# Kernel optimization log

Hardware: AMD Instinct MI355X
Metric: run time of the kernel (lower is better)

Reference implementation:

```python
import jax, jax.numpy as jnp
import numpy as np

D_MODEL = 1024
NUM_HEADS = 16

def _dense_params(key, d_in, d_out):
    kw, _ = jax.random.split(key)
    # flax default: lecun_normal kernel, zeros bias
    W = jax.random.normal(kw, (d_in, d_out), dtype=jnp.float32) / np.sqrt(d_in)
    b = jnp.zeros((d_out,), dtype=jnp.float32)
    return W, b

def setup_inputs() -> dict:
    key = jax.random.key(0)
    ks = jax.random.split(key, 8)
    B, Tx, Tc = 2, 2048, 2048
    x = jax.random.normal(ks[0], (B, Tx, D_MODEL), dtype=jnp.float32)
    context = jax.random.normal(ks[1], (B, Tc, D_MODEL), dtype=jnp.float32)
    Wq, bq = _dense_params(ks[2], D_MODEL, D_MODEL)
    Wks, bks = _dense_params(ks[3], D_MODEL, D_MODEL)
    Wvs, bvs = _dense_params(ks[4], D_MODEL, D_MODEL)
    Wkc, bkc = _dense_params(ks[5], D_MODEL, D_MODEL)
    Wvc, bvc = _dense_params(ks[6], D_MODEL, D_MODEL)
    Wo, bo = _dense_params(ks[7], D_MODEL, D_MODEL)
    return {"x": x, "context": context,
            "Wq": Wq, "bq": bq, "Wks": Wks, "bks": bks, "Wvs": Wvs, "bvs": bvs,
            "Wkc": Wkc, "bkc": bkc, "Wvc": Wvc, "bvc": bvc, "Wo": Wo, "bo": bo}

def _split_heads(t, H):
    B, T, C = t.shape
    return t.reshape(B, T, H, C // H).transpose(0, 2, 1, 3)  # [B,H,T,hd]

def reference(x, context, Wq, bq, Wks, bks, Wvs, bvs, Wkc, bkc, Wvc, bvc, Wo, bo):
    H = NUM_HEADS
    head_dim = D_MODEL // H
    q = x @ Wq + bq
    k = jnp.concatenate([x @ Wks + bks, context @ Wkc + bkc], axis=1)
    v = jnp.concatenate([x @ Wvs + bvs, context @ Wvc + bvc], axis=1)
    q = _split_heads(q, H)  # [B,H,Tq,hd]
    k = _split_heads(k, H)  # [B,H,Tk,hd]
    v = _split_heads(v, H)
    attn = jnp.einsum('bhqd,bhkd->bhqk', q, k) / jnp.sqrt(jnp.float32(head_dim))
    attn = jax.nn.softmax(attn, axis=-1)
    out = jnp.einsum('bhqk,bhkd->bhqd', attn, v)
    B, _, Tq, _ = out.shape
    out = out.transpose(0, 2, 1, 3).reshape(B, Tq, D_MODEL)
    return out @ Wo + bo
```

## Files before the change

kernel.cpp:

```cpp
#include <hip/hip_runtime.h>
#include <hip/hip_bf16.h>
#include <math.h>


typedef _Float16 f16;
typedef _Float16 f16x8 __attribute__((ext_vector_type(8)));
typedef _Float16 f16x4v __attribute__((ext_vector_type(4)));
typedef float    f32x4 __attribute__((ext_vector_type(4)));

#define MFMA_F16(a, b, c) __builtin_amdgcn_mfma_f32_16x16x32_f16((a), (b), (c), 0, 0, 0)

#define QSCALE 0.18033688011112042f

__device__ __forceinline__ void glds16(const f16* g, f16* l) {
    __builtin_amdgcn_global_load_lds(
        (const __attribute__((address_space(1))) void*)g,
        (__attribute__((address_space(3))) void*)l, 16, 0, 0);
}

__global__ __launch_bounds__(256) void prep(
    const float4* __restrict__ x, const float4* __restrict__ ctx,
    f16x4v* __restrict__ xb, f16x4v* __restrict__ cb,
    const float* __restrict__ W0, const float* __restrict__ W1,
    const float* __restrict__ W2, const float* __restrict__ W3,
    const float* __restrict__ W4, const float* __restrict__ W5,
    f16* __restrict__ wt)
{
    if (blockIdx.x < 8192) {
        const int n4 = (2 * 2048 * 1024) / 4;
        int i = blockIdx.x * 256 + threadIdx.x;
        float4 v;
        f16x4v* dst;
        if (i < n4) { v = x[i];        dst = xb + i; }
        else        { v = ctx[i - n4]; dst = cb + (i - n4); }
        f16x4v h = { (f16)v.x, (f16)v.y, (f16)v.z, (f16)v.w };
        *dst = h;
        return;
    }
    const int idx = blockIdx.x - 8192;
    const int z = idx >> 10, rem = idx & 1023;
    const float* Ws[6] = { W0, W1, W2, W3, W4, W5 };
    const float* W = Ws[z];
    f16* Wt = wt + (size_t)z * (1024 * 1024);

    __shared__ float tile[32][33];
    const int tx = threadIdx.x & 31, ty = threadIdx.x >> 5;
    const int n0 = (rem & 31) * 32, k0 = (rem >> 5) * 32;

#pragma unroll
    for (int i = 0; i < 4; ++i) {
        int r = i * 8 + ty;
        tile[r][tx] = W[(size_t)(k0 + r) * 1024 + n0 + tx];
    }
    __syncthreads();
#pragma unroll
    for (int i = 0; i < 4; ++i) {
        int r = i * 8 + ty;
        Wt[(size_t)(n0 + r) * 1024 + k0 + tx] = (f16)tile[tx][r];
    }
}

#define GEMM_PROLOGUE(BN)                                                     \
    const int m0 = blockIdx.x * 128, n0 = blockIdx.y * (BN);                  \
    const int tid = threadIdx.x;                                              \
    const int w = tid >> 6, lane = tid & 63, quad = lane >> 4, l15 = lane & 15;\
    const int wm = (w >> 1) * 64, wn = (w & 1) * ((BN) / 2);                  \
    const int qsw = (quad ^ ((l15 >> 1) & 3)) * 8;                            \
    int gA[2], gB[(BN) / 64];                                                 \
    _Pragma("unroll")                                                         \
    for (int p = 0; p < 2; ++p) {                                             \
        int s = tid + p * 256;                                                \
        int r = (s >> 2) & 127, c = (s & 3) ^ ((s >> 3) & 3);                 \
        gA[p] = (m0 + r) * 1024 + c * 8;                                      \
    }                                                                         \
    _Pragma("unroll")                                                         \
    for (int p = 0; p < (BN) / 64; ++p) {                                     \
        int s = tid + p * 256;                                                \
        int r = (s >> 2) & ((BN) - 1), c = (s & 3) ^ ((s >> 3) & 3);          \
        gB[p] = (n0 + r) * 1024 + c * 8;                                      \
    }

#define GEMM_STAGE(BN)                                                        \
    __syncthreads();                                                          \
    _Pragma("unroll")                                                         \
    for (int p = 0; p < 2; ++p) glds16(&A[gA[p] + k0], &As[(p * 256 + w * 64) * 8]); \
    _Pragma("unroll")                                                         \
    for (int p = 0; p < (BN) / 64; ++p) glds16(&Bt[gB[p] + k0], &Bs[(p * 256 + w * 64) * 8]); \
    __syncthreads();

__global__ __launch_bounds__(256) void proj_gemm(
    const f16* __restrict__ xb, const f16* __restrict__ cb,
    const f16* __restrict__ wt,
    const float* __restrict__ bq, const float* __restrict__ bks,
    const float* __restrict__ bkc, const float* __restrict__ bvs,
    const float* __restrict__ bvc,
    f16* __restrict__ qbuf, f16* __restrict__ kbuf, f16* __restrict__ vbuf)
{
    __shared__ alignas(16) f16 As[128 * 32];
    __shared__ alignas(16) f16 Bs[128 * 32];

    const int z = blockIdx.z;
    const f16* A = (z == 0 || z == 1 || z == 3) ? xb : cb;
    const int wslot = (z == 0) ? 0 : (z == 1) ? 1 : (z == 2) ? 3 : (z == 3) ? 2 : 4;
    const f16* Bt = wt + (size_t)wslot * 1048576;
    const float* bias = (z == 0) ? bq : (z == 1) ? bks : (z == 2) ? bkc
                        : (z == 3) ? bvs : bvc;
    const int roff = (z == 2 || z == 4) ? 2048 : 0;

    GEMM_PROLOGUE(128)
    f32x4 acc[4][4] = {};

    for (int k0 = 0; k0 < 1024; k0 += 32) {
        GEMM_STAGE(128)
        f16x8 a[4], b[4];
#pragma unroll
        for (int i = 0; i < 4; ++i)
            a[i] = *(const f16x8*)&As[(wm + i * 16 + l15) * 32 + qsw];
#pragma unroll
        for (int i = 0; i < 4; ++i)
            b[i] = *(const f16x8*)&Bs[(wn + i * 16 + l15) * 32 + qsw];
#pragma unroll
        for (int mi = 0; mi < 4; ++mi)
#pragma unroll
            for (int ni = 0; ni < 4; ++ni)
                acc[mi][ni] = MFMA_F16(a[mi], b[ni], acc[mi][ni]);
    }

#pragma unroll
    for (int mi = 0; mi < 4; ++mi) {
#pragma unroll
        for (int r = 0; r < 4; ++r) {
            int row = m0 + wm + mi * 16 + quad * 4 + r;
            int b_ = row >> 11, tok = row & 2047;
#pragma unroll
            for (int ni = 0; ni < 4; ++ni) {
                int col = n0 + wn + ni * 16 + l15;
                float v = acc[mi][ni][r] + bias[col];
                int bh = b_ * 16 + (col >> 6);
                int tg = roff + tok;
                if (z == 0) {
                    qbuf[((size_t)bh * 2048 + tok) * 64 + (col & 63)] = (f16)(v * QSCALE);
                } else if (z <= 2) {
                    kbuf[(size_t)bh * 262144 + (size_t)(tg >> 6) * 4096
                         + (size_t)((col >> 5) & 1) * 2048 + (tg & 63) * 32 + (col & 31)] = (f16)v;
                } else {
                    vbuf[(size_t)bh * 262144 + (size_t)tg * 64 + (col & 63)] = (f16)v;
                }
            }
        }
    }
}

__global__ __launch_bounds__(256) void transpose_v(
    const f16* __restrict__ vbuf, f16* __restrict__ vt)
{
    const int t = threadIdx.x;
    const int mt = t >> 3, md = t & 7;
    const int tok0 = blockIdx.x * 256 + mt * 8;
    const int z = blockIdx.y;
    f16x8 in[8];
#pragma unroll
    for (int i = 0; i < 8; ++i)
        in[i] = *(const f16x8*)&vbuf[((size_t)z * 4096 + tok0 + i) * 64 + md * 8];
    f16x8 ov[8];
#pragma unroll
    for (int j = 0; j < 8; ++j)
#pragma unroll
        for (int i = 0; i < 8; ++i) ov[j][i] = in[i][j];
    const int kt = tok0 >> 6, kks = (tok0 >> 5) & 1, kko = tok0 & 31;
#pragma unroll
    for (int j = 0; j < 8; ++j)
        *(f16x8*)&vt[(size_t)z * 262144 + (size_t)kt * 4096 + kks * 2048
                     + (md * 8 + j) * 32 + kko] = ov[j];
}

__global__ __launch_bounds__(256, 2) void attn_kernel(
    const f16* __restrict__ q, const f16* __restrict__ kb,
    const f16* __restrict__ vtb, f16* __restrict__ osplit,
    float* __restrict__ lsplit)
{
    __shared__ alignas(16) f16 K_lds[2][4096];
    __shared__ alignas(16) f16 V_lds[2][4096];
    __shared__ alignas(16) f16 P_lds[128 * 72];

    const int tid = threadIdx.x;
    const int w = tid >> 6, lane = tid & 63, quad = lane >> 4, l15 = lane & 15;
    const int bh = blockIdx.x, qt = blockIdx.y, sp = blockIdx.z;
    const int qbase = qt * 128;

    f16x8 qa[2][2];
#pragma unroll
    for (int nq = 0; nq < 2; ++nq) {
        const size_t qaddr =
            ((size_t)bh * 2048 + qbase + w * 32 + nq * 16 + l15) * 64 + quad * 8;
        qa[nq][0] = *(const f16x8*)&q[qaddr];
        qa[nq][1] = *(const f16x8*)&q[qaddr + 32];
    }

    f16x8 ones;
#pragma unroll
    for (int j = 0; j < 8; ++j) ones[j] = (f16)1.0f;

    f32x4 o_acc[2][4] = {};
    f32x4 l_acc[2] = {};

    const f16* ktile = kb + (size_t)bh * 262144 + (size_t)sp * 131072;
    const f16* vtile = vtb + (size_t)bh * 262144 + (size_t)sp * 131072;

    const int sco = ((tid >> 2) * 4 + ((tid & 3) ^ ((tid >> 3) & 3))) * 8;
    const int qsw = (quad ^ ((l15 >> 1) & 3)) * 8;
    const int wslot = w * 512;

    glds16(ktile + sco,        &K_lds[0][wslot]);
    glds16(ktile + 2048 + sco, &K_lds[0][2048 + wslot]);
    glds16(vtile + sco,        &V_lds[0][wslot]);
    glds16(vtile + 2048 + sco, &V_lds[0][2048 + wslot]);

    for (int kt = 0; kt < 32; ++kt) {
        const f16* Kc = K_lds[kt & 1];
        const f16* Vc = V_lds[kt & 1];
        f16* Kn = K_lds[(kt + 1) & 1];
        f16* Vn = V_lds[(kt + 1) & 1];

        __syncthreads();

        ktile += 4096; vtile += 4096;
        glds16(ktile + sco,        Kn + wslot);
        glds16(ktile + 2048 + sco, Kn + 2048 + wslot);
        glds16(vtile + sco,        Vn + wslot);
        glds16(vtile + 2048 + sco, Vn + 2048 + wslot);

        f32x4 s[4][2];
#pragma unroll
        for (int mt = 0; mt < 4; ++mt) {
            f16x8 ka0 = *(const f16x8*)&Kc[(mt * 16 + l15) * 32 + qsw];
            f16x8 ka1 = *(const f16x8*)&Kc[2048 + (mt * 16 + l15) * 32 + qsw];
#pragma unroll
            for (int nq = 0; nq < 2; ++nq) {
                f32x4 t = {};
                t = MFMA_F16(ka0, qa[nq][0], t);
                t = MFMA_F16(ka1, qa[nq][1], t);
                s[mt][nq] = t;
            }
        }

#pragma unroll
        for (int mt = 0; mt < 4; ++mt) {
#pragma unroll
            for (int nq = 0; nq < 2; ++nq) {
                f16x4v pk;
#pragma unroll
                for (int r = 0; r < 4; ++r)
                    pk[r] = (f16)__builtin_amdgcn_exp2f(s[mt][nq][r]);
                *(f16x4v*)&P_lds[(w * 32 + nq * 16 + l15) * 72 + mt * 16 + quad * 4] = pk;
            }
        }

        f16x8 pa[2][2];
#pragma unroll
        for (int nq = 0; nq < 2; ++nq)
#pragma unroll
            for (int ks = 0; ks < 2; ++ks)
                pa[nq][ks] = *(const f16x8*)&P_lds[(w * 32 + nq * 16 + l15) * 72 + ks * 32 + quad * 8];

#pragma unroll
        for (int nq = 0; nq < 2; ++nq) {
            l_acc[nq] = MFMA_F16(ones, pa[nq][0], l_acc[nq]);
            l_acc[nq] = MFMA_F16(ones, pa[nq][1], l_acc[nq]);
        }

#pragma unroll
        for (int dt = 0; dt < 4; ++dt) {
            f16x8 vb0 = *(const f16x8*)&Vc[(dt * 16 + l15) * 32 + qsw];
            f16x8 vb1 = *(const f16x8*)&Vc[2048 + (dt * 16 + l15) * 32 + qsw];
#pragma unroll
            for (int nq = 0; nq < 2; ++nq) {
                o_acc[nq][dt] = MFMA_F16(pa[nq][0], vb0, o_acc[nq][dt]);
                o_acc[nq][dt] = MFMA_F16(pa[nq][1], vb1, o_acc[nq][dt]);
            }
        }
    }

    const size_t sb = (size_t)(sp * 32 + bh) * 2048 + qbase;
#pragma unroll
    for (int nq = 0; nq < 2; ++nq) {
        if (quad == 0)
            lsplit[sb + w * 32 + nq * 16 + l15] = l_acc[nq][0];
#pragma unroll
        for (int r = 0; r < 4; ++r) {
            float lr = __shfl(l_acc[nq][0], quad * 4 + r, 64);
            float inv = 1.0f / lr;
            int ql = w * 32 + nq * 16 + quad * 4 + r;
            size_t obase = (sb + ql) * 64;
#pragma unroll
            for (int dt = 0; dt < 4; ++dt)
                osplit[obase + dt * 16 + l15] = (f16)(o_acc[nq][dt][r] * inv);
        }
    }
}

__global__ __launch_bounds__(256) void combine(
    const f16* __restrict__ osplit, const float* __restrict__ lsplit,
    f16* __restrict__ abuf)
{
    int idx = blockIdx.x * 256 + threadIdx.x;
    int d8 = idx & 7;
    int row = (idx >> 3) & 2047;
    int bh = idx >> 14;
    int b = bh >> 4, h = bh & 15;
    size_t base1 = ((size_t)bh * 2048 + row) * 64 + d8 * 8;
    size_t base2 = ((size_t)(32 + bh) * 2048 + row) * 64 + d8 * 8;
    float l1 = lsplit[bh * 2048 + row];
    float l2 = lsplit[(32 + bh) * 2048 + row];
    float inv = 1.0f / (l1 + l2);
    float w1 = l1 * inv, w2 = l2 * inv;
    f16x8 a = *(const f16x8*)&osplit[base1];
    f16x8 c = *(const f16x8*)&osplit[base2];
    f16x8 out;
#pragma unroll
    for (int j = 0; j < 8; ++j)
        out[j] = (f16)(w1 * (float)a[j] + w2 * (float)c[j]);
    *(f16x8*)&abuf[((size_t)(b * 2048 + row)) * 1024 + h * 64 + d8 * 8] = out;
}

__global__ __launch_bounds__(256) void out_gemm(
    const f16* __restrict__ abuf, const f16* __restrict__ wt5,
    const float* __restrict__ bo, float* __restrict__ out)
{
    __shared__ alignas(16) f16 As[128 * 32];
    __shared__ alignas(16) f16 Bs[64 * 32];

    const f16* A = abuf;
    const f16* Bt = wt5;

    GEMM_PROLOGUE(64)
    f32x4 acc[4][2] = {};

    for (int k0 = 0; k0 < 1024; k0 += 32) {
        GEMM_STAGE(64)
        f16x8 a[4], b[2];
#pragma unroll
        for (int i = 0; i < 4; ++i)
            a[i] = *(const f16x8*)&As[(wm + i * 16 + l15) * 32 + qsw];
#pragma unroll
        for (int i = 0; i < 2; ++i)
            b[i] = *(const f16x8*)&Bs[(wn + i * 16 + l15) * 32 + qsw];
#pragma unroll
        for (int mi = 0; mi < 4; ++mi)
#pragma unroll
            for (int ni = 0; ni < 2; ++ni)
                acc[mi][ni] = MFMA_F16(a[mi], b[ni], acc[mi][ni]);
    }

#pragma unroll
    for (int mi = 0; mi < 4; ++mi) {
#pragma unroll
        for (int r = 0; r < 4; ++r) {
            int row = m0 + wm + mi * 16 + quad * 4 + r;
#pragma unroll
            for (int ni = 0; ni < 2; ++ni) {
                int col = n0 + wn + ni * 16 + l15;
                out[(size_t)row * 1024 + col] = acc[mi][ni][r] + bo[col];
            }
        }
    }
}

extern "C" void kernel_launch(void* const* d_in, const int* in_sizes, int n_in,
                              void* d_out, int out_size, void* d_ws, size_t ws_size,
                              hipStream_t stream)
{
    (void)in_sizes; (void)n_in; (void)out_size; (void)ws_size;

    const float* x    = (const float*)d_in[0];
    const float* ctx  = (const float*)d_in[1];
    const float* Wq   = (const float*)d_in[2];  const float* bq  = (const float*)d_in[3];
    const float* Wks  = (const float*)d_in[4];  const float* bks = (const float*)d_in[5];
    const float* Wvs  = (const float*)d_in[6];  const float* bvs = (const float*)d_in[7];
    const float* Wkc  = (const float*)d_in[8];  const float* bkc = (const float*)d_in[9];
    const float* Wvc  = (const float*)d_in[10]; const float* bvc = (const float*)d_in[11];
    const float* Wo   = (const float*)d_in[12]; const float* bo  = (const float*)d_in[13];

    char* ws = (char*)d_ws;
    f16*   xb     = (f16*)(ws + 0);
    f16*   cb     = (f16*)(ws + 8388608);
    f16*   vt     = (f16*)(ws + 0);
    f16*   wt     = (f16*)(ws + 16777216);
    float* lsplit = (float*)(ws + 16777216);
    f16*   qbuf   = (f16*)(ws + 29360128);
    f16*   kbuf   = (f16*)(ws + 37748736);
    f16*   vbuf   = (f16*)(ws + 54525952);
    f16*   osplit = (f16*)(ws + 54525952);
    f16*   abuf   = (f16*)(ws + 71303168);

    prep<<<14336, 256, 0, stream>>>((const float4*)x, (const float4*)ctx,
                                    (f16x4v*)xb, (f16x4v*)cb,
                                    Wq, Wks, Wvs, Wkc, Wvc, Wo, wt);

    proj_gemm<<<dim3(32, 8, 5), 256, 0, stream>>>(
        xb, cb, wt, bq, bks, bkc, bvs, bvc, qbuf, kbuf, vbuf);

    transpose_v<<<dim3(16, 32), 256, 0, stream>>>(vbuf, vt);

    attn_kernel<<<dim3(32, 16, 2), 256, 0, stream>>>(qbuf, kbuf, vt, osplit, lsplit);

    combine<<<2048, 256, 0, stream>>>(osplit, lsplit, abuf);

    out_gemm<<<dim3(32, 16), 256, 0, stream>>>(abuf, wt + 5 * 1048576, bo, (float*)d_out);
}
```

Before: 318.7 us.

## Double-buffer LDS tiles in projection/output GEMMs and raise MFMA wave priority

The projection and output GEMMs now use two LDS buffers per operand. The next K-slice is issued via global_load_lds right after a single barrier, while MFMAs consume the current slice. This replaces the load-then-sync-then-compute pattern that left the math units idle during each tile fetch. The attention kernel also wraps its QK and PV MFMA blocks in s_setprio(1)/s_setprio(0) so waves in their matrix phase are favoured by the scheduler. The cost is doubled LDS use in the GEMMs, which may reduce occupancy.

```diff
diff --git a/kernel.cpp b/kernel.cpp
--- a/kernel.cpp
+++ b/kernel.cpp
@@ -80,13 +80,13 @@
         gB[p] = (n0 + r) * 1024 + c * 8;                                      \
     }
 
-#define GEMM_STAGE(BN)                                                        \
-    __syncthreads();                                                          \
+#define GEMM_STAGE_TO(BN, buf, koff)                                          \
     _Pragma("unroll")                                                         \
-    for (int p = 0; p < 2; ++p) glds16(&A[gA[p] + k0], &As[(p * 256 + w * 64) * 8]); \
+    for (int p = 0; p < 2; ++p)                                               \
+        glds16(&A[gA[p] + (koff)], &As[buf][(p * 256 + w * 64) * 8]);         \
     _Pragma("unroll")                                                         \
-    for (int p = 0; p < (BN) / 64; ++p) glds16(&Bt[gB[p] + k0], &Bs[(p * 256 + w * 64) * 8]); \
-    __syncthreads();
+    for (int p = 0; p < (BN) / 64; ++p)                                       \
+        glds16(&Bt[gB[p] + (koff)], &Bs[buf][(p * 256 + w * 64) * 8]);
 
 __global__ __launch_bounds__(256) void proj_gemm(
     const f16* __restrict__ xb, const f16* __restrict__ cb,
@@ -96,8 +96,8 @@
     const float* __restrict__ bvc,
     f16* __restrict__ qbuf, f16* __restrict__ kbuf, f16* __restrict__ vbuf)
 {
-    __shared__ alignas(16) f16 As[128 * 32];
-    __shared__ alignas(16) f16 Bs[128 * 32];
+    __shared__ alignas(16) f16 As[2][128 * 32];
+    __shared__ alignas(16) f16 Bs[2][128 * 32];
 
     const int z = blockIdx.z;
     const f16* A = (z == 0 || z == 1 || z == 3) ? xb : cb;
@@ -110,15 +110,21 @@
     GEMM_PROLOGUE(128)
     f32x4 acc[4][4] = {};
 
+    GEMM_STAGE_TO(128, 0, 0)
+
     for (int k0 = 0; k0 < 1024; k0 += 32) {
-        GEMM_STAGE(128)
+        const int cur = (k0 >> 5) & 1;
+        __syncthreads();
+        if (k0 + 32 < 1024) {
+            GEMM_STAGE_TO(128, cur ^ 1, k0 + 32)
+        }
         f16x8 a[4], b[4];
 #pragma unroll
         for (int i = 0; i < 4; ++i)
-            a[i] = *(const f16x8*)&As[(wm + i * 16 + l15) * 32 + qsw];
+            a[i] = *(const f16x8*)&As[cur][(wm + i * 16 + l15) * 32 + qsw];
 #pragma unroll
         for (int i = 0; i < 4; ++i)
-            b[i] = *(const f16x8*)&Bs[(wn + i * 16 + l15) * 32 + qsw];
+            b[i] = *(const f16x8*)&Bs[cur][(wn + i * 16 + l15) * 32 + qsw];
 #pragma unroll
         for (int mi = 0; mi < 4; ++mi)
 #pragma unroll
@@ -231,6 +237,7 @@
         glds16(vtile + 2048 + sco, Vn + 2048 + wslot);
 
         f32x4 s[4][2];
+        __builtin_amdgcn_s_setprio(1);
 #pragma unroll
         for (int mt = 0; mt < 4; ++mt) {
             f16x8 ka0 = *(const f16x8*)&Kc[(mt * 16 + l15) * 32 + qsw];
@@ -243,6 +250,7 @@
                 s[mt][nq] = t;
             }
         }
+        __builtin_amdgcn_s_setprio(0);
 
 #pragma unroll
         for (int mt = 0; mt < 4; ++mt) {
@@ -263,6 +271,7 @@
             for (int ks = 0; ks < 2; ++ks)
                 pa[nq][ks] = *(const f16x8*)&P_lds[(w * 32 + nq * 16 + l15) * 72 + ks * 32 + quad * 8];
 
+        __builtin_amdgcn_s_setprio(1);
 #pragma unroll
         for (int nq = 0; nq < 2; ++nq) {
             l_acc[nq] = MFMA_F16(ones, pa[nq][0], l_acc[nq]);
@@ -279,6 +288,7 @@
                 o_acc[nq][dt] = MFMA_F16(pa[nq][1], vb1, o_acc[nq][dt]);
             }
         }
+        __builtin_amdgcn_s_setprio(0);
     }
 
     const size_t sb = (size_t)(sp * 32 + bh) * 2048 + qbase;
@@ -327,8 +337,8 @@
     const f16* __restrict__ abuf, const f16* __restrict__ wt5,
     const float* __restrict__ bo, float* __restrict__ out)
 {
-    __shared__ alignas(16) f16 As[128 * 32];
-    __shared__ alignas(16) f16 Bs[64 * 32];
+    __shared__ alignas(16) f16 As[2][128 * 32];
+    __shared__ alignas(16) f16 Bs[2][64 * 32];
 
     const f16* A = abuf;
     const f16* Bt = wt5;
@@ -336,15 +346,21 @@
     GEMM_PROLOGUE(64)
     f32x4 acc[4][2] = {};
 
+    GEMM_STAGE_TO(64, 0, 0)
+
     for (int k0 = 0; k0 < 1024; k0 += 32) {
-        GEMM_STAGE(64)
+        const int cur = (k0 >> 5) & 1;
+        __syncthreads();
+        if (k0 + 32 < 1024) {
+            GEMM_STAGE_TO(64, cur ^ 1, k0 + 32)
+        }
         f16x8 a[4], b[2];
 #pragma unroll
         for (int i = 0; i < 4; ++i)
-            a[i] = *(const f16x8*)&As[(wm + i * 16 + l15) * 32 + qsw];
+            a[i] = *(const f16x8*)&As[cur][(wm + i * 16 + l15) * 32 + qsw];
 #pragma unroll
         for (int i = 0; i < 2; ++i)
-            b[i] = *(const f16x8*)&Bs[(wn + i * 16 + l15) * 32 + qsw];
+            b[i] = *(const f16x8*)&Bs[cur][(wn + i * 16 + l15) * 32 + qsw];
 #pragma unroll
         for (int mi = 0; mi < 4; ++mi)
 #pragma unroll
```

New measurement: 306.9 us. 3.7% less time.
